# Kernel tuning notes

Measured on AMD Instinct MI355X. Metric: run time of the kernel, lower is better.

## Reference

```python
import jax, jax.numpy as jnp
import numpy as np

N = 50000      # nodes
E = 800000     # edges (avg degree 16)
F_IN = 128     # num_node_features
H = 128        # hidden_dim
G = 500        # num graphs in batch


def setup_inputs() -> dict:
    key = jax.random.key(0)
    ks = jax.random.split(key, 20)
    inp = {
        "x": jax.random.normal(ks[0], (N, F_IN), dtype=jnp.float32),
        "edge_index": jax.random.randint(ks[1], (2, E), 0, N, dtype=jnp.int32),
        "batch": jnp.sort(jax.random.randint(ks[2], (N,), 0, G, dtype=jnp.int32)),
    }
    s = 0.05
    # 3 GIN layers: MLP = Linear -> ReLU -> Linear, plus learnable eps (init 0)
    dims = [(F_IN, H), (H, H), (H, H)]
    for i, (din, dout) in enumerate(dims):
        k = jax.random.split(ks[3 + i], 4)
        inp[f"W1_{i}"] = jax.random.normal(k[0], (din, H), dtype=jnp.float32) * s
        inp[f"b1_{i}"] = jnp.zeros((H,), dtype=jnp.float32)
        inp[f"W2_{i}"] = jax.random.normal(k[1], (H, dout), dtype=jnp.float32) * s
        inp[f"b2_{i}"] = jnp.zeros((dout,), dtype=jnp.float32)
        inp[f"eps_{i}"] = jnp.zeros((), dtype=jnp.float32)
    inp["fc_w"] = jax.random.normal(ks[10], (H, 1), dtype=jnp.float32) * s
    inp["fc_b"] = jnp.zeros((1,), dtype=jnp.float32)
    return inp


def _gin_layer(x, src, dst, eps, W1, b1, W2, b2):
    # neighbor sum: scatter-add messages x[src] into dst rows
    agg = jax.ops.segment_sum(x[src], dst, num_segments=N)  # [N, d]
    h = (1.0 + eps) * x + agg
    h = jax.nn.relu(h @ W1 + b1) @ W2 + b2
    return h


def reference(x, edge_index, batch,
              W1_0, b1_0, W2_0, b2_0, eps_0,
              W1_1, b1_1, W2_1, b2_1, eps_1,
              W1_2, b1_2, W2_2, b2_2, eps_2,
              fc_w, fc_b):
    src, dst = edge_index[0], edge_index[1]
    layers = [(eps_0, W1_0, b1_0, W2_0, b2_0),
              (eps_1, W1_1, b1_1, W2_1, b2_1),
              (eps_2, W1_2, b1_2, W2_2, b2_2)]
    h = x
    for i, (eps, W1, b1, W2, b2) in enumerate(layers):
        h = _gin_layer(h, src, dst, eps, W1, b1, W2, b2)
        if i < len(layers) - 1:
            h = jax.nn.relu(h)  # dropout is identity in eval mode
    # global mean pool over graph ids
    sums = jax.ops.segment_sum(h, batch, num_segments=G)          # [G, H]
    counts = jax.ops.segment_sum(jnp.ones((N,), h.dtype), batch, num_segments=G)
    pooled = sums / jnp.maximum(counts, 1.0)[:, None]
    out = pooled @ fc_w + fc_b  # [G, 1]
    return jnp.squeeze(out, axis=-1)  # [G]
```

## Files before the change

kernel.cpp:

```cpp
#include <hip/hip_runtime.h>


#define FEAT 128
#define BCAP 2048
#define CHUNK 10240

typedef short  bf16x8 __attribute__((ext_vector_type(8)));
typedef float  f32x4  __attribute__((ext_vector_type(4)));

__device__ inline unsigned short f2bf(float f) {
    unsigned int u = __float_as_uint(f);
    u = (u + 0x7FFFu + ((u >> 16) & 1u)) >> 16;
    return (unsigned short)u;
}
__device__ inline float2 bfpair(unsigned int u) {
    float2 r;
    r.x = __uint_as_float(u << 16);
    r.y = __uint_as_float(u & 0xffff0000u);
    return r;
}

__global__ __launch_bounds__(1024) void bucket_kernel(
    const int* __restrict__ src, const int* __restrict__ dst,
    int* __restrict__ bcnt, unsigned int* __restrict__ bpairs, int E) {
    __shared__ unsigned int lpairs[CHUNK];
    __shared__ int lbase[1025];
    __shared__ int lcur[1024];
    __shared__ int lres[1024];
    __shared__ int part[1024];
    int tid = threadIdx.x;
    int e0 = blockIdx.x * CHUNK;
    int e1 = e0 + CHUNK; if (e1 > E) e1 = E;
    int cnt = e1 - e0;
    lcur[tid] = 0;
    __syncthreads();
    for (int e = e0 + tid; e < e1; e += 1024) atomicAdd(&lcur[dst[e] >> 6], 1);
    __syncthreads();
    int v = lcur[tid];
    part[tid] = v;
    __syncthreads();
    for (int d = 1; d < 1024; d <<= 1) {
        int u = (tid >= d) ? part[tid - d] : 0;
        __syncthreads();
        part[tid] += u;
        __syncthreads();
    }
    int ex = part[tid] - v;
    lbase[tid] = ex;
    if (tid == 1023) lbase[1024] = part[1023];
    lcur[tid] = ex;
    lres[tid] = (v > 0) ? atomicAdd(&bcnt[tid * 16], v) : 0;
    __syncthreads();
    for (int e = e0 + tid; e < e1; e += 1024) {
        int d = dst[e], s = src[e];
        int p = atomicAdd(&lcur[d >> 6], 1);
        lpairs[p] = ((unsigned int)s << 6) | (unsigned int)(d & 63);
    }
    __syncthreads();
    for (int j = tid; j < cnt; j += 1024) {
        int lo = 0, hi = 1023;
        while (lo < hi) { int m = (lo + hi + 1) >> 1; if (lbase[m] <= j) lo = m; else hi = m - 1; }
        int gpos = lres[lo] + (j - lbase[lo]);
        if (gpos < BCAP) bpairs[(size_t)lo * BCAP + gpos] = lpairs[j];
    }
}

__global__ __launch_bounds__(256) void deg_kernel(const int* __restrict__ bcnt,
                                                  const unsigned int* __restrict__ bpairs,
                                                  int* __restrict__ off, int n) {
    __shared__ int lh[64];
    int b = blockIdx.x, tid = threadIdx.x;
    if (tid < 64) lh[tid] = 0;
    __syncthreads();
    int cnt = bcnt[b * 16]; if (cnt > BCAP) cnt = BCAP;
    const unsigned int* bp = bpairs + (size_t)b * BCAP;
    for (int i = tid; i < cnt; i += 256) atomicAdd(&lh[bp[i] & 63u], 1);
    __syncthreads();
    if (tid < 64) {
        int node = b * 64 + tid;
        if (node < n) off[node] = lh[tid];
    }
}

__global__ void block_sum_kernel(const int* __restrict__ off, int* __restrict__ bs, int n) {
    int b = blockIdx.x, t = threadIdx.x;
    int base = b * 1024;
    int s = 0;
    #pragma unroll
    for (int i = 0; i < 4; ++i) {
        int idx = base + t + 256 * i;
        if (idx < n) s += off[idx];
    }
    #pragma unroll
    for (int d = 32; d; d >>= 1) s += __shfl_down(s, d, 64);
    __shared__ int ws[4];
    if ((t & 63) == 0) ws[t >> 6] = s;
    __syncthreads();
    if (t == 0) bs[b] = ws[0] + ws[1] + ws[2] + ws[3];
}

__global__ void scan_blocksums_kernel(int* __restrict__ bs, int nb,
                                      int* __restrict__ off, int n) {
    __shared__ int l[1024];
    int t = threadIdx.x;
    int v = (t < nb) ? bs[t] : 0;
    l[t] = v;
    __syncthreads();
    for (int d = 1; d < 1024; d <<= 1) {
        int u = (t >= d) ? l[t - d] : 0;
        __syncthreads();
        l[t] += u;
        __syncthreads();
    }
    if (t < nb) bs[t] = (t == 0) ? 0 : l[t - 1];
    if (t == 1023) off[n] = l[1023];
}

__global__ __launch_bounds__(256) void block_scan_kernel(
    int* __restrict__ off, const int* __restrict__ bs, int n) {
    __shared__ int l[1024];
    __shared__ int part[256];
    int b = blockIdx.x, t = threadIdx.x;
    int base = b * 1024;
    #pragma unroll
    for (int i = 0; i < 4; ++i) {
        int idx = base + t + 256 * i;
        l[t + 256 * i] = (idx < n) ? off[idx] : 0;
    }
    __syncthreads();
    int v0 = l[4 * t], v1 = l[4 * t + 1], v2 = l[4 * t + 2], v3 = l[4 * t + 3];
    int p = v0 + v1 + v2 + v3;
    part[t] = p;
    __syncthreads();
    for (int d = 1; d < 256; d <<= 1) {
        int u = (t >= d) ? part[t - d] : 0;
        __syncthreads();
        part[t] += u;
        __syncthreads();
    }
    int ex = bs[b] + ((t == 0) ? 0 : part[t - 1]);
    int e0 = ex, e1 = ex + v0, e2 = e1 + v1, e3 = e2 + v2;
    int idx = base + 4 * t;
    if (idx + 3 < n) {
        ((int4*)(off + idx))[0] = make_int4(e0, e1, e2, e3);
    } else {
        if (idx + 0 < n) off[idx + 0] = e0;
        if (idx + 1 < n) off[idx + 1] = e1;
        if (idx + 2 < n) off[idx + 2] = e2;
    }
}

__global__ __launch_bounds__(256) void bucket_scatter_kernel(
    const int* __restrict__ bcnt, const unsigned int* __restrict__ bpairs,
    const int* __restrict__ off, int* __restrict__ srcs, int n) {
    __shared__ int lcur[64];
    int b = blockIdx.x, tid = threadIdx.x;
    if (tid < 64) {
        int node = b * 64 + tid;
        lcur[tid] = (node < n) ? off[node] : 0;
    }
    __syncthreads();
    int cnt = bcnt[b * 16]; if (cnt > BCAP) cnt = BCAP;
    const unsigned int* bp = bpairs + (size_t)b * BCAP;
    for (int i = tid; i < cnt; i += 256) {
        unsigned int pr = bp[i];
        int pos = atomicAdd(&lcur[pr & 63u], 1);
        srcs[pos] = (int)(pr >> 6);
    }
}

__global__ __launch_bounds__(256) void setup_kernel(
    const float* __restrict__ x, unsigned int* __restrict__ xbf, long pairs, int nxb,
    const int* __restrict__ batch, int* __restrict__ gstart, int n, int G,
    const float* __restrict__ W2f, const float* __restrict__ b2f,
    const float* __restrict__ fcw, float* __restrict__ weff,
    const float* __restrict__ W0, const float* __restrict__ W1,
    const float* __restrict__ W2, const float* __restrict__ W3,
    const float* __restrict__ W4, unsigned short* __restrict__ Wswz) {
    int b = blockIdx.x, tid = threadIdx.x;
    if (b < nxb) {
        long i = (long)b * 256 + tid;
        if (i < pairs) {
            float2 v = ((const float2*)x)[i];
            xbf[i] = (unsigned int)f2bf(v.x) | ((unsigned int)f2bf(v.y) << 16);
        }
    } else if (b < nxb + 2) {
        int i = (b - nxb) * 256 + tid;
        if (i <= G) {
            int lo = 0, hi = n;
            while (lo < hi) { int m = (lo + hi) >> 1; if (batch[m] < i) lo = m + 1; else hi = m; }
            gstart[i] = lo;
        }
    } else if (b == nxb + 2) {
        int lane = tid & 63, wave = tid >> 6;
        float2 f2 = ((const float2*)fcw)[lane];
        for (int r = wave; r < 128; r += 4) {
            float2 w = ((const float2*)(W2f + r * FEAT))[lane];
            float d = w.x * f2.x + w.y * f2.y;
            #pragma unroll
            for (int s = 32; s; s >>= 1) d += __shfl_down(d, s, 64);
            if (lane == 0) weff[r] = d;
        }
        if (wave == 0) {
            float2 bb = ((const float2*)b2f)[lane];
            float d = bb.x * f2.x + bb.y * f2.y;
            #pragma unroll
            for (int s = 32; s; s >>= 1) d += __shfl_down(d, s, 64);
            if (lane == 0) weff[128] = d;
        }
    } else {
        int gid = (b - nxb - 3) * 256 + tid;
        if (gid < 5 * 2048) {
            int mat = gid >> 11;
            int task = gid & 2047;
            int c = task >> 4, m = task & 15;
            const float* W = (mat == 0) ? W0 : (mat == 1) ? W1 : (mat == 2) ? W2 :
                             (mat == 3) ? W3 : W4;
            unsigned short* dp = Wswz + mat * 16384 + c * 128 + ((m ^ (c & 7)) << 3);
            #pragma unroll
            for (int j = 0; j < 8; ++j) dp[j] = f2bf(W[(8 * m + j) * FEAT + c]);
        }
    }
}

__global__ void agg_kernel(const unsigned int* __restrict__ h, const int* __restrict__ off,
                           const int* __restrict__ srcs, const float* __restrict__ eps_p,
                           unsigned int* __restrict__ pre_bf, int n) {
    int wave = (int)((blockIdx.x * (size_t)blockDim.x + threadIdx.x) >> 6);
    int lane = threadIdx.x & 63;
    if (wave >= n) return;
    float eps1 = 1.0f + eps_p[0];
    float2 self = bfpair(h[(size_t)wave * 64 + lane]);
    float2 acc0 = make_float2(self.x * eps1, self.y * eps1);
    float2 acc1 = make_float2(0.f, 0.f);
    float2 acc2 = make_float2(0.f, 0.f);
    float2 acc3 = make_float2(0.f, 0.f);
    int j0 = off[wave], j1 = off[wave + 1];
    int j = j0;
    for (; j + 8 <= j1; j += 8) {
        int s0 = srcs[j + 0], s1 = srcs[j + 1], s2 = srcs[j + 2], s3 = srcs[j + 3];
        int s4 = srcs[j + 4], s5 = srcs[j + 5], s6 = srcs[j + 6], s7 = srcs[j + 7];
        unsigned int u0 = h[(size_t)s0 * 64 + lane];
        unsigned int u1 = h[(size_t)s1 * 64 + lane];
        unsigned int u2 = h[(size_t)s2 * 64 + lane];
        unsigned int u3 = h[(size_t)s3 * 64 + lane];
        unsigned int u4 = h[(size_t)s4 * 64 + lane];
        unsigned int u5 = h[(size_t)s5 * 64 + lane];
        unsigned int u6 = h[(size_t)s6 * 64 + lane];
        unsigned int u7 = h[(size_t)s7 * 64 + lane];
        float2 v0 = bfpair(u0), v1 = bfpair(u1), v2 = bfpair(u2), v3 = bfpair(u3);
        float2 v4 = bfpair(u4), v5 = bfpair(u5), v6 = bfpair(u6), v7 = bfpair(u7);
        acc0.x += v0.x; acc0.y += v0.y;  acc1.x += v1.x; acc1.y += v1.y;
        acc2.x += v2.x; acc2.y += v2.y;  acc3.x += v3.x; acc3.y += v3.y;
        acc0.x += v4.x; acc0.y += v4.y;  acc1.x += v5.x; acc1.y += v5.y;
        acc2.x += v6.x; acc2.y += v6.y;  acc3.x += v7.x; acc3.y += v7.y;
    }
    for (; j < j1; ++j) {
        int s = srcs[j];
        float2 v = bfpair(h[(size_t)s * 64 + lane]);
        acc0.x += v.x; acc0.y += v.y;
    }
    acc0.x += acc1.x + acc2.x + acc3.x;
    acc0.y += acc1.y + acc2.y + acc3.y;
    pre_bf[(size_t)wave * 64 + lane] =
        (unsigned int)f2bf(acc0.x) | ((unsigned int)f2bf(acc0.y) << 16);
}

template <int MODE>
__global__ __launch_bounds__(256) void mfma_mlp_kernel(
    const unsigned short* __restrict__ A, const unsigned short* __restrict__ Wswz,
    const float* __restrict__ bias, unsigned short* __restrict__ outbf,
    const int* __restrict__ batch, const float* __restrict__ weff,
    float* __restrict__ sums, int n) {
    __shared__ int4 Wl4[2048];
    int tid = threadIdx.x;
    const int4* ws4 = (const int4*)Wswz;
    #pragma unroll
    for (int i = 0; i < 8; ++i) Wl4[i * 256 + tid] = ws4[i * 256 + tid];
    __syncthreads();
    const unsigned short* Wl = (const unsigned short*)Wl4;

    int lane = tid & 63, wave = tid >> 6;
    int q = lane >> 4, c15 = lane & 15;
    int r0 = blockIdx.x * 64 + wave * 16;
    int arow = r0 + c15;
    bool rv = arow < n;
    const bf16x8* ap = (const bf16x8*)(A + (size_t)arow * FEAT + q * 8);

    f32x4 zf = {0.f, 0.f, 0.f, 0.f};
    f32x4 acc[8];
    #pragma unroll
    for (int i = 0; i < 8; ++i) acc[i] = zf;
    bf16x8 zero8 = {0, 0, 0, 0, 0, 0, 0, 0};

    #pragma unroll
    for (int k0 = 0; k0 < 4; ++k0) {
        bf16x8 a = rv ? ap[k0 * 4] : zero8;
        int m = k0 * 4 + q;
        #pragma unroll
        for (int nt = 0; nt < 8; ++nt) {
            int col = nt * 16 + c15;
            bf16x8 b = *(const bf16x8*)&Wl[col * 128 + ((m ^ (col & 7)) << 3)];
            acc[nt] = __builtin_amdgcn_mfma_f32_16x16x32_bf16(a, b, acc[nt], 0, 0, 0);
        }
    }

    int orow0 = r0 + q * 4;
    if (MODE == 1) {
        #pragma unroll
        for (int nt = 0; nt < 8; ++nt) {
            int col = nt * 16 + c15;
            float bv = bias[col];
            #pragma unroll
            for (int r = 0; r < 4; ++r) {
                int ro = orow0 + r;
                if (ro < n) {
                    float v = fmaxf(acc[nt][r] + bv, 0.f);
                    outbf[(size_t)ro * FEAT + col] = f2bf(v);
                }
            }
        }
    } else {
        __shared__ float gsum[64];
        int r0b = blockIdx.x * 64;
        int lastn = r0b + 63 < n - 1 ? r0b + 63 : n - 1;
        int gmin = batch[r0b];
        int gmax = batch[lastn];
        int span = gmax - gmin + 1;
        bool lds_ok = (span <= 64);
        if (lds_ok) for (int i = tid; i < span; i += 256) gsum[i] = 0.f;
        __syncthreads();
        float rowdot[4] = {0.f, 0.f, 0.f, 0.f};
        #pragma unroll
        for (int nt = 0; nt < 8; ++nt) {
            int col = nt * 16 + c15;
            float bv = bias[col];
            float wv = weff[col];
            #pragma unroll
            for (int r = 0; r < 4; ++r)
                rowdot[r] += fmaxf(acc[nt][r] + bv, 0.f) * wv;
        }
        #pragma unroll
        for (int r = 0; r < 4; ++r) {
            float v = rowdot[r];
            v += __shfl_xor(v, 1, 64);
            v += __shfl_xor(v, 2, 64);
            v += __shfl_xor(v, 4, 64);
            v += __shfl_xor(v, 8, 64);
            if (c15 == 0) {
                int node = orow0 + r;
                if (node < n) {
                    int g = batch[node];
                    if (lds_ok) atomicAdd(&gsum[g - gmin], v);
                    else        atomicAdd(&sums[g], v);
                }
            }
        }
        __syncthreads();
        if (lds_ok)
            for (int i = tid; i < span; i += 256) atomicAdd(&sums[gmin + i], gsum[i]);
    }
}

__global__ void finalize_kernel(const float* __restrict__ sums, const int* __restrict__ gstart,
                                const float* __restrict__ weff, const float* __restrict__ fcb,
                                float* __restrict__ out, int G) {
    int g = blockIdx.x * blockDim.x + threadIdx.x;
    if (g >= G) return;
    int cnt = gstart[g + 1] - gstart[g];
    out[g] = (cnt > 0) ? sums[g] / (float)cnt + weff[128] + fcb[0] : fcb[0];
}

static inline size_t align256(size_t x) { return (x + 255) & ~(size_t)255; }

extern "C" void kernel_launch(void* const* d_in, const int* in_sizes, int n_in,
                              void* d_out, int out_size, void* d_ws, size_t ws_size,
                              hipStream_t stream) {
    const float* x      = (const float*)d_in[0];
    const int*   ei     = (const int*)d_in[1];
    const int*   batch  = (const int*)d_in[2];
    const float* W1[3]  = {(const float*)d_in[3],  (const float*)d_in[8],  (const float*)d_in[13]};
    const float* b1[3]  = {(const float*)d_in[4],  (const float*)d_in[9],  (const float*)d_in[14]};
    const float* W2[3]  = {(const float*)d_in[5],  (const float*)d_in[10], (const float*)d_in[15]};
    const float* b2[3]  = {(const float*)d_in[6],  (const float*)d_in[11], (const float*)d_in[16]};
    const float* eps[3] = {(const float*)d_in[7],  (const float*)d_in[12], (const float*)d_in[17]};
    const float* fcw    = (const float*)d_in[18];
    const float* fcb    = (const float*)d_in[19];
    float* out = (float*)d_out;

    const int N = in_sizes[0] / FEAT;
    const int E = in_sizes[1] / 2;
    const int G = out_size;
    const int nbuckets = (N + 63) >> 6;

    char* p = (char*)d_ws;
    int* off    = (int*)p;  p += align256((size_t)(N + 1) * 4);
    int* srcs   = (int*)p;  p += align256((size_t)E * 4);
    int* bsums  = (int*)p;  p += align256((size_t)1024 * 4);
    int* gstart = (int*)p;  p += align256((size_t)(G + 1) * 4);
    float* weff = (float*)p; p += align256((size_t)256 * 4);
    unsigned short* Wswz = (unsigned short*)p; p += align256((size_t)5 * 16384 * 2);
    float* sums = (float*)p;
    char* z0 = (char*)sums;
    p += align256((size_t)G * 4);
    int* bcnt = (int*)p; p += align256((size_t)nbuckets * 16 * 4);
    size_t zbytes = (size_t)(p - z0);
    unsigned int* bpairs = (unsigned int*)p;     p += align256((size_t)nbuckets * BCAP * 4);
    unsigned int* x_bf   = (unsigned int*)p;     p += align256((size_t)N * 64 * 4);
    unsigned int* pre_bf = (unsigned int*)p;     p += align256((size_t)N * 64 * 4);
    unsigned int* t_bf   = (unsigned int*)p;     p += align256((size_t)N * 64 * 4);
    unsigned int* h_bf   = (unsigned int*)p;     p += align256((size_t)N * 64 * 4);
    (void)ws_size; (void)n_in;

    const int* src = ei;
    const int* dst = ei + E;

    hipMemsetAsync(z0, 0, zbytes, stream);

    const int nb = (N + 1023) / 1024;
    const int nchunks = (E + CHUNK - 1) / CHUNK;
    bucket_kernel<<<nchunks, 1024, 0, stream>>>(src, dst, bcnt, bpairs, E);
    deg_kernel<<<nbuckets, 256, 0, stream>>>(bcnt, bpairs, off, N);
    block_sum_kernel<<<nb, 256, 0, stream>>>(off, bsums, N);
    scan_blocksums_kernel<<<1, 1024, 0, stream>>>(bsums, nb, off, N);
    block_scan_kernel<<<nb, 256, 0, stream>>>(off, bsums, N);
    bucket_scatter_kernel<<<nbuckets, 256, 0, stream>>>(bcnt, bpairs, off, srcs, N);

    long pairs = (long)N * 64;
    int nxb = (int)((pairs + 255) / 256);
    setup_kernel<<<nxb + 43, 256, 0, stream>>>(
        x, x_bf, pairs, nxb, batch, gstart, N, G,
        W2[2], b2[2], fcw, weff,
        W1[0], W2[0], W1[1], W2[1], W1[2], Wswz);

    const int aggBlocks  = (N + 3) / 4;
    const int gemmBlocks = (N + 63) / 64;
    const unsigned short* Wz[5] = {Wswz, Wswz + 16384, Wswz + 2 * 16384,
                                   Wswz + 3 * 16384, Wswz + 4 * 16384};

    const unsigned int* h = x_bf;
    for (int i = 0; i < 2; ++i) {
        agg_kernel<<<aggBlocks, 256, 0, stream>>>(h, off, srcs, eps[i], pre_bf, N);
        mfma_mlp_kernel<1><<<gemmBlocks, 256, 0, stream>>>(
            (const unsigned short*)pre_bf, Wz[2 * i], b1[i], (unsigned short*)t_bf,
            nullptr, nullptr, nullptr, N);
        mfma_mlp_kernel<1><<<gemmBlocks, 256, 0, stream>>>(
            (const unsigned short*)t_bf, Wz[2 * i + 1], b2[i], (unsigned short*)h_bf,
            nullptr, nullptr, nullptr, N);
        h = h_bf;
    }
    agg_kernel<<<aggBlocks, 256, 0, stream>>>(h, off, srcs, eps[2], pre_bf, N);
    mfma_mlp_kernel<2><<<gemmBlocks, 256, 0, stream>>>(
        (const unsigned short*)pre_bf, Wz[4], b1[2], nullptr,
        batch, weff, sums, N);

    finalize_kernel<<<(G + 255) / 256, 256, 0, stream>>>(sums, gstart, weff, fcb, out, G);
}
```

Baseline: 324.5 us.

## Store node features in feature-sliced layout so gathers stay cache-resident per slice

Node features are stored as 8 slices of 16 bf16 features (32 bytes per node per slice) instead of full 256-byte rows. The aggregation kernel assigns each block to one slice, so each gather pass touches a 1.6 MB working set that fits better in L2. The MFMA kernels read and write this sliced layout. In exchange, every gathered segment is only 32 bytes wide, which is less efficient per transaction and needs more blocks and more index loads per feature.

```diff
diff --git a/kernel.cpp b/kernel.cpp
--- a/kernel.cpp
+++ b/kernel.cpp
@@ -182,7 +182,11 @@
         long i = (long)b * 256 + tid;
         if (i < pairs) {
             float2 v = ((const float2*)x)[i];
-            xbf[i] = (unsigned int)f2bf(v.x) | ((unsigned int)f2bf(v.y) << 16);
+            unsigned int pk = (unsigned int)f2bf(v.x) | ((unsigned int)f2bf(v.y) << 16);
+            long node = i >> 6;
+            int dg = (int)(i & 63);
+            int slice = dg >> 3, d = dg & 7;
+            xbf[(size_t)slice * n * 8 + node * 8 + d] = pk;
         }
     } else if (b < nxb + 2) {
         int i = (b - nxb) * 256 + tid;
@@ -223,46 +227,47 @@
     }
 }
 
-__global__ void agg_kernel(const unsigned int* __restrict__ h, const int* __restrict__ off,
-                           const int* __restrict__ srcs, const float* __restrict__ eps_p,
-                           unsigned int* __restrict__ pre_bf, int n) {
-    int wave = (int)((blockIdx.x * (size_t)blockDim.x + threadIdx.x) >> 6);
-    int lane = threadIdx.x & 63;
-    if (wave >= n) return;
+__global__ __launch_bounds__(256) void agg_kernel(
+    const unsigned int* __restrict__ hs, const int* __restrict__ off,
+    const int* __restrict__ srcs, const float* __restrict__ eps_p,
+    unsigned int* __restrict__ pre, int n) {
+    int b = blockIdx.x;
+    int slice = b & 7;
+    int chunk = b >> 3;
+    int tid = threadIdx.x;
+    int wave = tid >> 6, lane = tid & 63;
+    int g = lane >> 3, d = lane & 7;
+    int node = chunk * 32 + wave * 8 + g;
+    if (node >= n) return;
     float eps1 = 1.0f + eps_p[0];
-    float2 self = bfpair(h[(size_t)wave * 64 + lane]);
+    const unsigned int* hb = hs + (size_t)slice * n * 8;
+    float2 self = bfpair(hb[(size_t)node * 8 + d]);
     float2 acc0 = make_float2(self.x * eps1, self.y * eps1);
     float2 acc1 = make_float2(0.f, 0.f);
     float2 acc2 = make_float2(0.f, 0.f);
     float2 acc3 = make_float2(0.f, 0.f);
-    int j0 = off[wave], j1 = off[wave + 1];
+    int j0 = off[node], j1 = off[node + 1];
     int j = j0;
-    for (; j + 8 <= j1; j += 8) {
-        int s0 = srcs[j + 0], s1 = srcs[j + 1], s2 = srcs[j + 2], s3 = srcs[j + 3];
-        int s4 = srcs[j + 4], s5 = srcs[j + 5], s6 = srcs[j + 6], s7 = srcs[j + 7];
-        unsigned int u0 = h[(size_t)s0 * 64 + lane];
-        unsigned int u1 = h[(size_t)s1 * 64 + lane];
-        unsigned int u2 = h[(size_t)s2 * 64 + lane];
-        unsigned int u3 = h[(size_t)s3 * 64 + lane];
-        unsigned int u4 = h[(size_t)s4 * 64 + lane];
-        unsigned int u5 = h[(size_t)s5 * 64 + lane];
-        unsigned int u6 = h[(size_t)s6 * 64 + lane];
-        unsigned int u7 = h[(size_t)s7 * 64 + lane];
+    for (; j + 4 <= j1; j += 4) {
+        int s0 = srcs[j], s1 = srcs[j + 1], s2 = srcs[j + 2], s3 = srcs[j + 3];
+        unsigned int u0 = hb[(size_t)s0 * 8 + d];
+        unsigned int u1 = hb[(size_t)s1 * 8 + d];
+        unsigned int u2 = hb[(size_t)s2 * 8 + d];
+        unsigned int u3 = hb[(size_t)s3 * 8 + d];
         float2 v0 = bfpair(u0), v1 = bfpair(u1), v2 = bfpair(u2), v3 = bfpair(u3);
-        float2 v4 = bfpair(u4), v5 = bfpair(u5), v6 = bfpair(u6), v7 = bfpair(u7);
         acc0.x += v0.x; acc0.y += v0.y;  acc1.x += v1.x; acc1.y += v1.y;
         acc2.x += v2.x; acc2.y += v2.y;  acc3.x += v3.x; acc3.y += v3.y;
-        acc0.x += v4.x; acc0.y += v4.y;  acc1.x += v5.x; acc1.y += v5.y;
-        acc2.x += v6.x; acc2.y += v6.y;  acc3.x += v7.x; acc3.y += v7.y;
     }
     for (; j < j1; ++j) {
         int s = srcs[j];
-        float2 v = bfpair(h[(size_t)s * 64 + lane]);
+        float2 v = bfpair(hb[(size_t)s * 8 + d]);
         acc0.x += v.x; acc0.y += v.y;
     }
-    acc0.x += acc1.x + acc2.x + acc3.x;
-    acc0.y += acc1.y + acc2.y + acc3.y;
-    pre_bf[(size_t)wave * 64 + lane] =
+    acc0.x += acc1.x + acc2.x;
+    acc0.y += acc1.y + acc2.y;
+    acc0.x += acc3.x;
+    acc0.y += acc3.y;
+    pre[(size_t)slice * n * 8 + (size_t)node * 8 + d] =
         (unsigned int)f2bf(acc0.x) | ((unsigned int)f2bf(acc0.y) << 16);
 }
 
@@ -285,7 +290,8 @@
     int r0 = blockIdx.x * 64 + wave * 16;
     int arow = r0 + c15;
     bool rv = arow < n;
-    const bf16x8* ap = (const bf16x8*)(A + (size_t)arow * FEAT + q * 8);
+    size_t sstride = (size_t)n * 16;
+    const unsigned short* abase = A + (size_t)arow * 16 + 8 * (q & 1) + (q >> 1) * sstride;
 
     f32x4 zf = {0.f, 0.f, 0.f, 0.f};
     f32x4 acc[8];
@@ -295,13 +301,13 @@
 
     #pragma unroll
     for (int k0 = 0; k0 < 4; ++k0) {
-        bf16x8 a = rv ? ap[k0 * 4] : zero8;
+        bf16x8 a = rv ? *(const bf16x8*)(abase + 2 * k0 * sstride) : zero8;
         int m = k0 * 4 + q;
         #pragma unroll
         for (int nt = 0; nt < 8; ++nt) {
             int col = nt * 16 + c15;
-            bf16x8 b = *(const bf16x8*)&Wl[col * 128 + ((m ^ (col & 7)) << 3)];
-            acc[nt] = __builtin_amdgcn_mfma_f32_16x16x32_bf16(a, b, acc[nt], 0, 0, 0);
+            bf16x8 bfr = *(const bf16x8*)&Wl[col * 128 + ((m ^ (col & 7)) << 3)];
+            acc[nt] = __builtin_amdgcn_mfma_f32_16x16x32_bf16(a, bfr, acc[nt], 0, 0, 0);
         }
     }
 
@@ -309,14 +315,13 @@
     if (MODE == 1) {
         #pragma unroll
         for (int nt = 0; nt < 8; ++nt) {
-            int col = nt * 16 + c15;
-            float bv = bias[col];
+            float bv = bias[nt * 16 + c15];
             #pragma unroll
             for (int r = 0; r < 4; ++r) {
                 int ro = orow0 + r;
                 if (ro < n) {
                     float v = fmaxf(acc[nt][r] + bv, 0.f);
-                    outbf[(size_t)ro * FEAT + col] = f2bf(v);
+                    outbf[(size_t)nt * sstride + (size_t)ro * 16 + c15] = f2bf(v);
                 }
             }
         }
@@ -433,7 +438,7 @@
         W2[2], b2[2], fcw, weff,
         W1[0], W2[0], W1[1], W2[1], W1[2], Wswz);
 
-    const int aggBlocks  = (N + 3) / 4;
+    const int aggBlocks  = 8 * ((N + 31) / 32);
     const int gemmBlocks = (N + 63) / 64;
     const unsigned short* Wz[5] = {Wswz, Wswz + 16384, Wswz + 2 * 16384,
                                    Wswz + 3 * 16384, Wswz + 4 * 16384};
```

Measured after the change: 335.8 us. +3.5%, slower.
